# Performance work log

Hardware: AMD Instinct MI355X
Metric: run time of the kernel (lower is better)

The kernel has to match this reference:

```python
import math
import jax, jax.numpy as jnp
import numpy as np

B, Q, L, H = 32, 40, 1024, 1024
WINDOW_FRAMES, MAX_V_L = 16, 1024
MAX_DELTA = 0.1
NUM_PASSES = 2


def setup_inputs() -> dict:
    key = jax.random.key(0)
    ks = jax.random.split(key, 8)
    init_log_sigma = math.log(WINDOW_FRAMES / (2.0 * MAX_V_L))
    return {
        "pred_spans": jax.random.uniform(ks[0], (B, Q, 2), dtype=jnp.float32),
        "vid_feat": jax.random.normal(ks[1], (B, L, H), dtype=jnp.float32),
        "vid_mask": jnp.ones((B, L), dtype=jnp.float32),
        "txt_rep": jax.random.normal(ks[2], (B, H), dtype=jnp.float32),
        "log_sigma_start": jnp.float32(init_log_sigma),
        "log_sigma_end": jnp.float32(init_log_sigma),
        "sigma_width_scale_start": jnp.float32(0.01),
        "sigma_width_scale_end": jnp.float32(-0.01),
        "txt_proj_w": jax.random.normal(ks[3], (H, 2), dtype=jnp.float32) * 0.02,
        "txt_proj_b": jnp.zeros((2,), dtype=jnp.float32),
        "mlp0_w": jax.random.normal(ks[4], (3 * H, H), dtype=jnp.float32) * (1.0 / math.sqrt(3 * H)),
        "mlp0_b": jnp.zeros((H,), dtype=jnp.float32),
        "mlp1_w": jax.random.normal(ks[5], (H, 2), dtype=jnp.float32) * (1.0 / math.sqrt(H)),
        "mlp1_b": jnp.zeros((2,), dtype=jnp.float32),
    }


def reference(pred_spans, vid_feat, vid_mask, txt_rep,
              log_sigma_start, log_sigma_end,
              sigma_width_scale_start, sigma_width_scale_end,
              txt_proj_w, txt_proj_b, mlp0_w, mlp0_b, mlp1_w, mlp1_b):
    b, q, _ = pred_spans.shape
    l = vid_feat.shape[1]
    # span (center,width) -> (start,end) in [0,1]
    start = jnp.clip(pred_spans[..., 0] - pred_spans[..., 1] / 2, 0.0, 1.0)  # (B,Q)
    end = jnp.clip(pred_spans[..., 0] + pred_spans[..., 1] / 2, 0.0, 1.0)
    t_pos = jnp.linspace(0.0, 1.0, l)  # (L,)
    min_sig = 1.0 / (4.0 * l)
    log_range = math.log(max(float(l) * min_sig * 4.0, 1.0 + 1e-6))
    # semantic sigma offsets (B,2)
    txt_off = jnp.tanh(txt_rep @ txt_proj_w + txt_proj_b) * (0.5 * log_range)
    txt_off_s, txt_off_e = txt_off[:, 0:1], txt_off[:, 1:2]  # (B,1)
    txt_expand = jnp.broadcast_to(txt_rep[:, None, :], (b, q, txt_rep.shape[-1]))
    mask = vid_mask[:, None, :]  # (B,1,L)

    def _pool(anchor, sigma):
        # Gaussian soft-attention pooling over frames; anchor,sigma: (B,Q)
        dist2 = ((t_pos[None, None, :] - anchor[:, :, None]) / sigma[:, :, None]) ** 2
        w = jnp.exp(-0.5 * dist2) * mask  # (B,Q,L)
        w = w / jnp.maximum(jnp.sum(w, -1, keepdims=True), 1e-8)
        return jnp.einsum('bql,blh->bqh', w, vid_feat)

    passes = []
    for _ in range(NUM_PASSES):
        width = jnp.maximum(end - start, 1e-6)  # (B,Q)
        sig_s = jnp.maximum(jnp.exp(log_sigma_start + sigma_width_scale_start * width + txt_off_s), min_sig)
        sig_e = jnp.maximum(jnp.exp(log_sigma_end + sigma_width_scale_end * width + txt_off_e), min_sig)
        start_feat = _pool(start, sig_s)
        end_feat = _pool(end, sig_e)
        joint = jnp.concatenate([start_feat, end_feat, txt_expand], axis=-1)  # (B,Q,3H)
        hidden = jax.nn.relu(joint @ mlp0_w + mlp0_b)
        deltas = jnp.tanh(hidden @ mlp1_w + mlp1_b) * MAX_DELTA  # (B,Q,2)
        start = jnp.clip(start + deltas[..., 0], 0.0, 1.0)
        end = jnp.clip(end + deltas[..., 1], 0.0, 1.0)
        center_r = (start + end) / 2.0
        width_r = jnp.maximum(end - start, 1e-6)
        passes.append(jnp.stack([center_r, width_r], axis=-1))
    return passes[-1], jnp.stack(passes, axis=0)
```

## Files before the change

kernel.cpp:

```cpp
#include <hip/hip_runtime.h>

#define B_   32
#define Q_   40
#define L_   1024
#define H_   1024
#define QQ_  80
#define M_   1280
#define K3_  3072
#define JK_  2048

#define OB_W0T   0u
#define OB_WT2   6291456u
#define OB_JOINT 11534336u
#define OB_PART  16777216u
#define OB_TXTB  27262976u
#define OB_TXTP  27328512u
#define OB_MISC  27590656u
#define MS_START 0
#define MS_END   1280
#define MS_TOS   2560
#define MS_TOE   2592

typedef short bf8 __attribute__((ext_vector_type(8)));
typedef short bf4 __attribute__((ext_vector_type(4)));
typedef float f4  __attribute__((ext_vector_type(4)));

static __device__ __forceinline__ unsigned short f2b(float f) {
    unsigned int x = __float_as_uint(f);
    unsigned int r = x + 0x7FFFu + ((x >> 16) & 1u);
    return (unsigned short)(r >> 16);
}
static __device__ __forceinline__ unsigned int pk2(float lo, float hi) {
    return (unsigned int)f2b(lo) | ((unsigned int)f2b(hi) << 16);
}
static __device__ __forceinline__ float b2f16(unsigned short u) {
    return __uint_as_float((unsigned int)u << 16);
}
static __device__ __forceinline__ float blo(unsigned int u) {
    return __uint_as_float(u << 16);
}
static __device__ __forceinline__ float bhi(unsigned int u) {
    return __uint_as_float(u & 0xffff0000u);
}

static __device__ __forceinline__ void block_reduce2(float& a, float& b, float* scr) {
    #pragma unroll
    for (int off = 32; off > 0; off >>= 1) {
        a += __shfl_down(a, off);
        b += __shfl_down(b, off);
    }
    int wv = threadIdx.x >> 6, lane = threadIdx.x & 63;
    __syncthreads();
    if (lane == 0) { scr[wv] = a; scr[4 + wv] = b; }
    __syncthreads();
    a = scr[0] + scr[1] + scr[2] + scr[3];
    b = scr[4] + scr[5] + scr[6] + scr[7];
}

__global__ __launch_bounds__(256) void k_setup(const float* __restrict__ w0,
                                               unsigned short* __restrict__ w0t,
                                               const float* __restrict__ txt,
                                               const float* __restrict__ pw,
                                               const float* __restrict__ pb,
                                               const float* __restrict__ spans,
                                               unsigned short* __restrict__ txtb,
                                               float* __restrict__ msc) {
    int z = blockIdx.z, tid = threadIdx.x;
    if (z == 3) {
        int flat = blockIdx.x * 16 + blockIdx.y;
        if (flat < B_) {
            int b = flat;
            int h4 = tid * 4;
            float4 tv = *(const float4*)(txt + (size_t)b * H_ + h4);
            float4 pa = *(const float4*)(pw + 2 * h4);
            float4 pc = *(const float4*)(pw + 2 * h4 + 4);
            float s0 = tv.x * pa.x + tv.y * pa.z + tv.z * pc.x + tv.w * pc.z;
            float s1 = tv.x * pa.y + tv.y * pa.w + tv.z * pc.y + tv.w * pc.w;
            ushort4 o;
            o.x = f2b(tv.x); o.y = f2b(tv.y); o.z = f2b(tv.z); o.w = f2b(tv.w);
            *(ushort4*)(txtb + (size_t)b * H_ + h4) = o;
            __shared__ float scr[8];
            block_reduce2(s0, s1, scr);
            if (tid == 0) {
                const float half_lr = 4.9999975e-07f;
                msc[MS_TOS + b] = tanhf(s0 + pb[0]) * half_lr;
                msc[MS_TOE + b] = tanhf(s1 + pb[1]) * half_lr;
            }
        } else if (flat < 37) {
            int i = (flat - B_) * 256 + tid;
            if (i < M_) {
                float c = spans[2 * i], w = spans[2 * i + 1];
                msc[MS_START + i] = fminf(fmaxf(c - 0.5f * w, 0.f), 1.f);
                msc[MS_END + i]   = fminf(fmaxf(c + 0.5f * w, 0.f), 1.f);
            }
        }
        return;
    }
    __shared__ float tile[64][69];
    const float* s = w0 + (size_t)z * 1024 * H_;
    unsigned short* d = w0t + (size_t)z * 1024;
    int r0 = blockIdx.x * 64, c0 = blockIdx.y * 64;
    int col4 = (tid & 15) * 4, row = tid >> 4;
    #pragma unroll
    for (int it = 0; it < 4; it++) {
        int r = it * 16 + row;
        float4 v = *(const float4*)(s + (size_t)(r0 + r) * 1024 + c0 + col4);
        *(float4*)(&tile[r][col4]) = v;
    }
    __syncthreads();
    #pragma unroll
    for (int it = 0; it < 2; it++) {
        int slot = it * 256 + tid;
        int c = slot >> 3, chunk = slot & 7;
        int r = chunk * 8;
        uint4 vv;
        vv.x = (unsigned int)f2b(tile[r + 0][c]) | ((unsigned int)f2b(tile[r + 1][c]) << 16);
        vv.y = (unsigned int)f2b(tile[r + 2][c]) | ((unsigned int)f2b(tile[r + 3][c]) << 16);
        vv.z = (unsigned int)f2b(tile[r + 4][c]) | ((unsigned int)f2b(tile[r + 5][c]) << 16);
        vv.w = (unsigned int)f2b(tile[r + 6][c]) | ((unsigned int)f2b(tile[r + 7][c]) << 16);
        *(uint4*)(d + (size_t)(c0 + c) * K3_ + r0 + r) = vv;
    }
}

static __device__ __forceinline__ void weights_body(int m, float s, float e,
                                                    const float* __restrict__ vmask,
                                                    float ls_s, float ls_e,
                                                    float sw_s, float sw_e,
                                                    const float* __restrict__ msc,
                                                    unsigned short* __restrict__ wt2,
                                                    float* scr) {
    int b = m / Q_, q = m - b * Q_;
    int tid = threadIdx.x;
    float width = fmaxf(e - s, 1e-6f);
    const float min_sig = 1.0f / (4.0f * (float)L_);
    float sig_s = fmaxf(expf(ls_s + sw_s * width + msc[MS_TOS + b]), min_sig);
    float sig_e = fmaxf(expf(ls_e + sw_e * width + msc[MS_TOE + b]), min_sig);
    float inv_s = 1.0f / sig_s, inv_e = 1.0f / sig_e;

    float wsv[4], wev[4], sumS = 0.f, sumE = 0.f;
    #pragma unroll
    for (int k = 0; k < 4; k++) {
        int l = tid + k * 256;
        float t = (float)l * (1.0f / 1023.0f);
        float mk = vmask[b * L_ + l];
        float ds = (t - s) * inv_s, de = (t - e) * inv_e;
        float a = expf(-0.5f * ds * ds) * mk;
        float c = expf(-0.5f * de * de) * mk;
        wsv[k] = a; wev[k] = c; sumS += a; sumE += c;
    }
    block_reduce2(sumS, sumE, scr);
    float iS = 1.0f / fmaxf(sumS, 1e-8f);
    float iE = 1.0f / fmaxf(sumE, 1e-8f);
    unsigned short* wq = wt2 + ((size_t)b * QQ_ + q) * L_;
    unsigned short* we = wt2 + ((size_t)b * QQ_ + Q_ + q) * L_;
    #pragma unroll
    for (int k = 0; k < 4; k++) {
        int l = tid + k * 256;
        wq[l] = f2b(wsv[k] * iS);
        we[l] = f2b(wev[k] * iE);
    }
}

__global__ __launch_bounds__(256) void k_stage2(const float* __restrict__ vmask,
                                                const float* __restrict__ p_ls_s,
                                                const float* __restrict__ p_ls_e,
                                                const float* __restrict__ p_sw_s,
                                                const float* __restrict__ p_sw_e,
                                                const float* __restrict__ msc,
                                                unsigned short* __restrict__ wt2,
                                                const unsigned short* __restrict__ txtb,
                                                const unsigned short* __restrict__ w0t,
                                                unsigned short* __restrict__ txtp) {
    int bid = blockIdx.x;
    if (bid < M_) {
        __shared__ float scr[8];
        int m = bid;
        weights_body(m, msc[MS_START + m], msc[MS_END + m], vmask,
                     p_ls_s[0], p_ls_e[0], p_sw_s[0], p_sw_e[0], msc, wt2, scr);
        return;
    }
    int t = bid - M_;
    int nIdx = t & 15, mIdx = (t >> 4) & 1, kIdx = t >> 5;
    int wv = threadIdx.x >> 6, lane = threadIdx.x & 63;
    int ml = lane & 15, kg = lane >> 4;
    int mbase = mIdx * 16;
    int nbase = nIdx * 64 + wv * 16;
    int kz = kIdx * 256;
    const unsigned short* ap = txtb + ((size_t)(mbase + ml) * H_ + kz + kg * 8);
    const unsigned short* bp = w0t + ((size_t)(nbase + ml) * K3_ + JK_ + kz + kg * 8);
    f4 acc = (f4){0.f, 0.f, 0.f, 0.f};
    #pragma unroll
    for (int k0 = 0; k0 < 256; k0 += 32) {
        bf8 a = *(const bf8*)(ap + k0);
        bf8 bb = *(const bf8*)(bp + k0);
        acc = __builtin_amdgcn_mfma_f32_16x16x32_bf16(a, bb, acc, 0, 0, 0);
    }
    unsigned short* pp = txtp + (size_t)kIdx * B_ * H_;
    int n = nbase + ml;
    #pragma unroll
    for (int r = 0; r < 4; r++) {
        int m = mbase + kg * 4 + r;
        pp[(size_t)m * H_ + n] = f2b(acc[r]);
    }
}

__global__ __launch_bounds__(256) void k_pool_mfma(const float* __restrict__ vid,
                                                   const unsigned short* __restrict__ wt2,
                                                   unsigned short* __restrict__ joint) {
    int b = blockIdx.x, ht = blockIdx.y;
    int tid = threadIdx.x;
    int hsub = tid >> 6, lane = tid & 63;
    int ml = lane & 15, kg = lane >> 4;
    int h0 = ht * 64;

    __shared__ __align__(16) unsigned short tb[2][4096];
    __shared__ __align__(16) unsigned short ta[2][80 * 72];

    int l0 = tid >> 3;
    int h8 = (tid & 7) * 8;
    int sB = (l0 >> 2) & 1, kgB = l0 >> 3, lrB = l0 & 3;
    int h16 = h8 >> 4, hc = h8 & 15;
    int b_off = ((((h16) * 2 + sB) * 4 + kgB) * 64) + lrB * 16 + hc;
    const float* vbase = vid + (size_t)b * L_ * H_ + h0 + h8;

    const unsigned short* awsrc = wt2 + (size_t)b * QQ_ * L_;

    f4 acc[5];
    #pragma unroll
    for (int t = 0; t < 5; t++) acc[t] = (f4){0.f, 0.f, 0.f, 0.f};

    float4 pv0, pv1, pv2, pv3;
    uint4 av0, av1, av2;

    auto issueB = [&](int c) {
        const float* src = vbase + (size_t)(c * 64 + l0) * H_;
        pv0 = *(const float4*)(src);
        pv1 = *(const float4*)(src + 4);
        pv2 = *(const float4*)(src + 32 * H_);
        pv3 = *(const float4*)(src + 32 * H_ + 4);
    };
    auto issueA = [&](int c) {
        int i0 = tid, i1 = tid + 256;
        av0 = *(const uint4*)(awsrc + (size_t)(i0 >> 3) * L_ + c * 64 + (i0 & 7) * 8);
        av1 = *(const uint4*)(awsrc + (size_t)(i1 >> 3) * L_ + c * 64 + (i1 & 7) * 8);
        if (tid < 128) {
            int i2 = tid + 512;
            av2 = *(const uint4*)(awsrc + (size_t)(i2 >> 3) * L_ + c * 64 + (i2 & 7) * 8);
        }
    };
    auto writeStage = [&](int buf) {
        uint4 w;
        w.x = pk2(pv0.x, pv0.y); w.y = pk2(pv0.z, pv0.w);
        w.z = pk2(pv1.x, pv1.y); w.w = pk2(pv1.z, pv1.w);
        *(uint4*)(&tb[buf][b_off]) = w;
        uint4 w2;
        w2.x = pk2(pv2.x, pv2.y); w2.y = pk2(pv2.z, pv2.w);
        w2.z = pk2(pv3.x, pv3.y); w2.w = pk2(pv3.z, pv3.w);
        *(uint4*)(&tb[buf][b_off + 2048]) = w2;
        int i0 = tid, i1 = tid + 256;
        *(uint4*)(&ta[buf][(i0 >> 3) * 72 + (i0 & 7) * 8]) = av0;
        *(uint4*)(&ta[buf][(i1 >> 3) * 72 + (i1 & 7) * 8]) = av1;
        if (tid < 128) {
            int i2 = tid + 512;
            *(uint4*)(&ta[buf][(i2 >> 3) * 72 + (i2 & 7) * 8]) = av2;
        }
    };

    issueB(0); issueA(0);
    writeStage(0);
    __syncthreads();

    for (int c = 0; c < 16; c++) {
        int buf = c & 1;
        if (c < 15) { issueB(c + 1); issueA(c + 1); }

        #pragma unroll
        for (int s2 = 0; s2 < 2; s2++) {
            unsigned trb = (unsigned)(uintptr_t)(&tb[buf][0]) + (s2 * 4 + hsub) * 1024
                           + lane * 8;
            bf4 lo, hi;
            asm volatile("ds_read_b64_tr_b16 %0, %2\n\t"
                         "ds_read_b64_tr_b16 %1, %2 offset:512\n\t"
                         "s_waitcnt lgkmcnt(0)"
                         : "=v"(lo), "=v"(hi)
                         : "v"(trb));
            __builtin_amdgcn_sched_barrier(0);
            bf8 bfrag = __builtin_shufflevector(lo, hi, 0, 1, 2, 3, 4, 5, 6, 7);
            #pragma unroll
            for (int t = 0; t < 5; t++) {
                bf8 afr = *(const bf8*)(&ta[buf][(t * 16 + ml) * 72 + s2 * 32 + kg * 8]);
                acc[t] = __builtin_amdgcn_mfma_f32_16x16x32_bf16(afr, bfrag, acc[t], 0, 0, 0);
            }
        }

        if (c < 15) writeStage(buf ^ 1);
        __syncthreads();
    }

    #pragma unroll
    for (int t = 0; t < 5; t++) {
        #pragma unroll
        for (int r = 0; r < 4; r++) {
            int qq = t * 16 + kg * 4 + r;
            int row = b * Q_ + (qq >= Q_ ? qq - Q_ : qq);
            int col = (qq >= Q_ ? H_ : 0) + h0 + hsub * 16 + ml;
            joint[(size_t)row * JK_ + col] = f2b(acc[t][r]);
        }
    }
}

__global__ __launch_bounds__(256) void k_mlp0_mfma(const unsigned short* __restrict__ joint,
                                                   const unsigned short* __restrict__ w0t,
                                                   const unsigned short* __restrict__ txtp,
                                                   unsigned short* __restrict__ part) {
    int wv = threadIdx.x >> 6, lane = threadIdx.x & 63;
    int ml = lane & 15, kg = lane >> 4;
    int mbase = blockIdx.x * 64 + wv * 16;
    int nbase = blockIdx.y * 64;
    int kbase = blockIdx.z * 512;
    const unsigned short* ap = joint + ((size_t)(mbase + ml) * JK_ + kbase + kg * 8);
    const unsigned short* bp = w0t + ((size_t)(nbase + ml) * K3_ + kbase + kg * 8);
    f4 acc[4];
    #pragma unroll
    for (int t = 0; t < 4; t++) acc[t] = (f4){0.f, 0.f, 0.f, 0.f};

    #pragma unroll 4
    for (int k0 = 0; k0 < 512; k0 += 32) {
        bf8 a = *(const bf8*)(ap + k0);
        #pragma unroll
        for (int t = 0; t < 4; t++) {
            bf8 bb = *(const bf8*)(bp + (size_t)t * 16 * K3_ + k0);
            acc[t] = __builtin_amdgcn_mfma_f32_16x16x32_bf16(a, bb, acc[t], 0, 0, 0);
        }
    }
    const unsigned short* tp = txtp + (size_t)blockIdx.z * B_ * H_;
    unsigned short* pp = part + (size_t)blockIdx.z * M_ * H_;
    #pragma unroll
    for (int t = 0; t < 4; t++) {
        int n = nbase + t * 16 + ml;
        #pragma unroll
        for (int r = 0; r < 4; r++) {
            int m = mbase + kg * 4 + r;
            int b = m / Q_;
            float v = acc[t][r] + b2f16(tp[(size_t)b * H_ + n]);
            pp[(size_t)m * H_ + n] = f2b(v);
        }
    }
}

__global__ __launch_bounds__(256) void k_mlp1w(const float* __restrict__ w1,
                                               const float* __restrict__ b0,
                                               const float* __restrict__ b1,
                                               const unsigned short* __restrict__ part,
                                               float* __restrict__ msc,
                                               float* __restrict__ out, int pass,
                                               int do_weights,
                                               const float* __restrict__ vmask,
                                               const float* __restrict__ p_ls_s,
                                               const float* __restrict__ p_ls_e,
                                               const float* __restrict__ p_sw_s,
                                               const float* __restrict__ p_sw_e,
                                               unsigned short* __restrict__ wt2) {
    int m = blockIdx.x, tid = threadIdx.x;
    int k4 = tid * 4;
    float4 bb = *(const float4*)(b0 + k4);
    float h0 = bb.x, h1 = bb.y, h2 = bb.z, h3 = bb.w;
    #pragma unroll
    for (int z = 0; z < 4; z++) {
        uint2 u = *(const uint2*)(part + (size_t)z * M_ * H_ + (size_t)m * H_ + k4);
        h0 += blo(u.x); h1 += bhi(u.x);
        h2 += blo(u.y); h3 += bhi(u.y);
    }
    h0 = fmaxf(h0, 0.f); h1 = fmaxf(h1, 0.f);
    h2 = fmaxf(h2, 0.f); h3 = fmaxf(h3, 0.f);
    float4 wa = *(const float4*)(w1 + 2 * k4);
    float4 wb = *(const float4*)(w1 + 2 * k4 + 4);
    float p0 = h0 * wa.x + h1 * wa.z + h2 * wb.x + h3 * wb.z;
    float p1 = h0 * wa.y + h1 * wa.w + h2 * wb.y + h3 * wb.w;

    __shared__ float scr[8];
    __shared__ float sh_s, sh_e;
    block_reduce2(p0, p1, scr);
    if (tid == 0) {
        float d0 = tanhf(p0 + b1[0]) * 0.1f;
        float d1 = tanhf(p1 + b1[1]) * 0.1f;
        float s = fminf(fmaxf(msc[MS_START + m] + d0, 0.f), 1.f);
        float e = fminf(fmaxf(msc[MS_END + m] + d1, 0.f), 1.f);
        msc[MS_START + m] = s;
        msc[MS_END + m] = e;
        sh_s = s; sh_e = e;
        float cen = 0.5f * (s + e);
        float wid = fmaxf(e - s, 1e-6f);
        out[2560 + (size_t)(pass * M_ + m) * 2 + 0] = cen;
        out[2560 + (size_t)(pass * M_ + m) * 2 + 1] = wid;
        if (pass == 1) { out[2 * m + 0] = cen; out[2 * m + 1] = wid; }
    }
    __syncthreads();
    if (do_weights) {
        weights_body(m, sh_s, sh_e, vmask,
                     p_ls_s[0], p_ls_e[0], p_sw_s[0], p_sw_e[0], msc, wt2, scr);
    }
}

extern "C" void kernel_launch(void* const* d_in, const int* in_sizes, int n_in,
                              void* d_out, int out_size, void* d_ws, size_t ws_size,
                              hipStream_t stream) {
    const float* spans = (const float*)d_in[0];
    const float* vid   = (const float*)d_in[1];
    const float* vmask = (const float*)d_in[2];
    const float* txt   = (const float*)d_in[3];
    const float* ls_s  = (const float*)d_in[4];
    const float* ls_e  = (const float*)d_in[5];
    const float* sw_s  = (const float*)d_in[6];
    const float* sw_e  = (const float*)d_in[7];
    const float* pw    = (const float*)d_in[8];
    const float* pb    = (const float*)d_in[9];
    const float* w0    = (const float*)d_in[10];
    const float* b0    = (const float*)d_in[11];
    const float* w1    = (const float*)d_in[12];
    const float* b1    = (const float*)d_in[13];
    char* wsb = (char*)d_ws;
    unsigned short* w0t   = (unsigned short*)(wsb + OB_W0T);
    unsigned short* wt2   = (unsigned short*)(wsb + OB_WT2);
    unsigned short* joint = (unsigned short*)(wsb + OB_JOINT);
    unsigned short* part  = (unsigned short*)(wsb + OB_PART);
    unsigned short* txtb  = (unsigned short*)(wsb + OB_TXTB);
    unsigned short* txtp  = (unsigned short*)(wsb + OB_TXTP);
    float* msc = (float*)(wsb + OB_MISC);
    float* out = (float*)d_out;

    hipLaunchKernelGGL(k_setup, dim3(16, 16, 4), dim3(256), 0, stream,
                       w0, w0t, txt, pw, pb, spans, txtb, msc);
    hipLaunchKernelGGL(k_stage2, dim3(M_ + 128), dim3(256), 0, stream,
                       vmask, ls_s, ls_e, sw_s, sw_e, msc, wt2, txtb, w0t, txtp);
    for (int p = 0; p < 2; p++) {
        hipLaunchKernelGGL(k_pool_mfma, dim3(B_, 16), dim3(256), 0, stream, vid, wt2, joint);
        hipLaunchKernelGGL(k_mlp0_mfma, dim3(20, 16, 4), dim3(256), 0, stream,
                           joint, w0t, txtp, part);
        hipLaunchKernelGGL(k_mlp1w, dim3(M_), dim3(256), 0, stream,
                           w1, b0, b1, part, msc, out, p, (p == 0) ? 1 : 0,
                           vmask, ls_s, ls_e, sw_s, sw_e, wt2);
    }
}
```

Measured before the change: 365.1 us.

## Fold stage2 into setup and first pool launch to drop a kernel

Removes the separate k_stage2 launch. The first-pass Gaussian weight computation moves into k_setup as extra z-slices, which recompute the text projection and span clipping locally. The txt@W0 partial GEMM moves into extra blockIdx.y rows of the first pool launch. This saves one launch and its serialization point, at the cost of redundant per-block text projection work and heavier setup and pool grids. Correctness depends on w0t and txtb being written by the earlier setup launch.

```diff
diff --git a/kernel.cpp b/kernel.cpp
--- a/kernel.cpp
+++ b/kernel.cpp
@@ -57,6 +57,57 @@
     b = scr[4] + scr[5] + scr[6] + scr[7];
 }
 
+static __device__ __forceinline__ void weights_core(int m, float s, float e,
+                                                    float toff_s, float toff_e,
+                                                    const float* __restrict__ vmask,
+                                                    float ls_s, float ls_e,
+                                                    float sw_s, float sw_e,
+                                                    unsigned short* __restrict__ wt2,
+                                                    float* scr) {
+    int b = m / Q_, q = m - b * Q_;
+    int tid = threadIdx.x;
+    float width = fmaxf(e - s, 1e-6f);
+    const float min_sig = 1.0f / (4.0f * (float)L_);
+    float sig_s = fmaxf(expf(ls_s + sw_s * width + toff_s), min_sig);
+    float sig_e = fmaxf(expf(ls_e + sw_e * width + toff_e), min_sig);
+    float inv_s = 1.0f / sig_s, inv_e = 1.0f / sig_e;
+
+    float wsv[4], wev[4], sumS = 0.f, sumE = 0.f;
+    #pragma unroll
+    for (int k = 0; k < 4; k++) {
+        int l = tid + k * 256;
+        float t = (float)l * (1.0f / 1023.0f);
+        float mk = vmask[b * L_ + l];
+        float ds = (t - s) * inv_s, de = (t - e) * inv_e;
+        float a = expf(-0.5f * ds * ds) * mk;
+        float c = expf(-0.5f * de * de) * mk;
+        wsv[k] = a; wev[k] = c; sumS += a; sumE += c;
+    }
+    block_reduce2(sumS, sumE, scr);
+    float iS = 1.0f / fmaxf(sumS, 1e-8f);
+    float iE = 1.0f / fmaxf(sumE, 1e-8f);
+    unsigned short* wq = wt2 + ((size_t)b * QQ_ + q) * L_;
+    unsigned short* we = wt2 + ((size_t)b * QQ_ + Q_ + q) * L_;
+    #pragma unroll
+    for (int k = 0; k < 4; k++) {
+        int l = tid + k * 256;
+        wq[l] = f2b(wsv[k] * iS);
+        we[l] = f2b(wev[k] * iE);
+    }
+}
+
+static __device__ __forceinline__ void weights_body(int m, float s, float e,
+                                                    const float* __restrict__ vmask,
+                                                    float ls_s, float ls_e,
+                                                    float sw_s, float sw_e,
+                                                    const float* __restrict__ msc,
+                                                    unsigned short* __restrict__ wt2,
+                                                    float* scr) {
+    int b = m / Q_;
+    weights_core(m, s, e, msc[MS_TOS + b], msc[MS_TOE + b],
+                 vmask, ls_s, ls_e, sw_s, sw_e, wt2, scr);
+}
+
 __global__ __launch_bounds__(256) void k_setup(const float* __restrict__ w0,
                                                unsigned short* __restrict__ w0t,
                                                const float* __restrict__ txt,
@@ -64,8 +115,35 @@
                                                const float* __restrict__ pb,
                                                const float* __restrict__ spans,
                                                unsigned short* __restrict__ txtb,
-                                               float* __restrict__ msc) {
+                                               float* __restrict__ msc,
+                                               const float* __restrict__ vmask,
+                                               const float* __restrict__ p_ls_s,
+                                               const float* __restrict__ p_ls_e,
+                                               const float* __restrict__ p_sw_s,
+                                               const float* __restrict__ p_sw_e,
+                                               unsigned short* __restrict__ wt2) {
     int z = blockIdx.z, tid = threadIdx.x;
+    if (z >= 4) {
+        int m = (z - 4) * 256 + (blockIdx.x * 16 + blockIdx.y);
+        int b = m / Q_;
+        int h4 = tid * 4;
+        float4 tv = *(const float4*)(txt + (size_t)b * H_ + h4);
+        float4 pa = *(const float4*)(pw + 2 * h4);
+        float4 pc = *(const float4*)(pw + 2 * h4 + 4);
+        float s0 = tv.x * pa.x + tv.y * pa.z + tv.z * pc.x + tv.w * pc.z;
+        float s1 = tv.x * pa.y + tv.y * pa.w + tv.z * pc.y + tv.w * pc.w;
+        __shared__ float scrW[8];
+        block_reduce2(s0, s1, scrW);
+        const float half_lr = 4.9999975e-07f;
+        float toff_s = tanhf(s0 + pb[0]) * half_lr;
+        float toff_e = tanhf(s1 + pb[1]) * half_lr;
+        float c = spans[2 * m], w = spans[2 * m + 1];
+        float s = fminf(fmaxf(c - 0.5f * w, 0.f), 1.f);
+        float e = fminf(fmaxf(c + 0.5f * w, 0.f), 1.f);
+        weights_core(m, s, e, toff_s, toff_e, vmask,
+                     p_ls_s[0], p_ls_e[0], p_sw_s[0], p_sw_e[0], wt2, scrW);
+        return;
+    }
     if (z == 3) {
         int flat = blockIdx.x * 16 + blockIdx.y;
         if (flat < B_) {
@@ -122,91 +200,39 @@
     }
 }
 
-static __device__ __forceinline__ void weights_body(int m, float s, float e,
-                                                    const float* __restrict__ vmask,
-                                                    float ls_s, float ls_e,
-                                                    float sw_s, float sw_e,
-                                                    const float* __restrict__ msc,
-                                                    unsigned short* __restrict__ wt2,
-                                                    float* scr) {
-    int b = m / Q_, q = m - b * Q_;
-    int tid = threadIdx.x;
-    float width = fmaxf(e - s, 1e-6f);
-    const float min_sig = 1.0f / (4.0f * (float)L_);
-    float sig_s = fmaxf(expf(ls_s + sw_s * width + msc[MS_TOS + b]), min_sig);
-    float sig_e = fmaxf(expf(ls_e + sw_e * width + msc[MS_TOE + b]), min_sig);
-    float inv_s = 1.0f / sig_s, inv_e = 1.0f / sig_e;
-
-    float wsv[4], wev[4], sumS = 0.f, sumE = 0.f;
-    #pragma unroll
-    for (int k = 0; k < 4; k++) {
-        int l = tid + k * 256;
-        float t = (float)l * (1.0f / 1023.0f);
-        float mk = vmask[b * L_ + l];
-        float ds = (t - s) * inv_s, de = (t - e) * inv_e;
-        float a = expf(-0.5f * ds * ds) * mk;
-        float c = expf(-0.5f * de * de) * mk;
-        wsv[k] = a; wev[k] = c; sumS += a; sumE += c;
-    }
-    block_reduce2(sumS, sumE, scr);
-    float iS = 1.0f / fmaxf(sumS, 1e-8f);
-    float iE = 1.0f / fmaxf(sumE, 1e-8f);
-    unsigned short* wq = wt2 + ((size_t)b * QQ_ + q) * L_;
-    unsigned short* we = wt2 + ((size_t)b * QQ_ + Q_ + q) * L_;
-    #pragma unroll
-    for (int k = 0; k < 4; k++) {
-        int l = tid + k * 256;
-        wq[l] = f2b(wsv[k] * iS);
-        we[l] = f2b(wev[k] * iE);
-    }
-}
-
-__global__ __launch_bounds__(256) void k_stage2(const float* __restrict__ vmask,
-                                                const float* __restrict__ p_ls_s,
-                                                const float* __restrict__ p_ls_e,
-                                                const float* __restrict__ p_sw_s,
-                                                const float* __restrict__ p_sw_e,
-                                                const float* __restrict__ msc,
-                                                unsigned short* __restrict__ wt2,
-                                                const unsigned short* __restrict__ txtb,
-                                                const unsigned short* __restrict__ w0t,
-                                                unsigned short* __restrict__ txtp) {
-    int bid = blockIdx.x;
-    if (bid < M_) {
-        __shared__ float scr[8];
-        int m = bid;
-        weights_body(m, msc[MS_START + m], msc[MS_END + m], vmask,
-                     p_ls_s[0], p_ls_e[0], p_sw_s[0], p_sw_e[0], msc, wt2, scr);
-        return;
-    }
-    int t = bid - M_;
-    int nIdx = t & 15, mIdx = (t >> 4) & 1, kIdx = t >> 5;
-    int wv = threadIdx.x >> 6, lane = threadIdx.x & 63;
-    int ml = lane & 15, kg = lane >> 4;
-    int mbase = mIdx * 16;
-    int nbase = nIdx * 64 + wv * 16;
-    int kz = kIdx * 256;
-    const unsigned short* ap = txtb + ((size_t)(mbase + ml) * H_ + kz + kg * 8);
-    const unsigned short* bp = w0t + ((size_t)(nbase + ml) * K3_ + JK_ + kz + kg * 8);
-    f4 acc = (f4){0.f, 0.f, 0.f, 0.f};
-    #pragma unroll
-    for (int k0 = 0; k0 < 256; k0 += 32) {
-        bf8 a = *(const bf8*)(ap + k0);
-        bf8 bb = *(const bf8*)(bp + k0);
-        acc = __builtin_amdgcn_mfma_f32_16x16x32_bf16(a, bb, acc, 0, 0, 0);
-    }
-    unsigned short* pp = txtp + (size_t)kIdx * B_ * H_;
-    int n = nbase + ml;
-    #pragma unroll
-    for (int r = 0; r < 4; r++) {
-        int m = mbase + kg * 4 + r;
-        pp[(size_t)m * H_ + n] = f2b(acc[r]);
-    }
-}
-
 __global__ __launch_bounds__(256) void k_pool_mfma(const float* __restrict__ vid,
                                                    const unsigned short* __restrict__ wt2,
-                                                   unsigned short* __restrict__ joint) {
+                                                   unsigned short* __restrict__ joint,
+                                                   const unsigned short* __restrict__ txtb,
+                                                   const unsigned short* __restrict__ w0t,
+                                                   unsigned short* __restrict__ txtp) {
+    if (blockIdx.y >= 16) {
+        int t = (blockIdx.y - 16) * 32 + blockIdx.x;
+        int nIdx = t & 15, mIdx = (t >> 4) & 1, kIdx = t >> 5;
+        int wv = threadIdx.x >> 6, lane = threadIdx.x & 63;
+        int ml = lane & 15, kg = lane >> 4;
+        int mbase = mIdx * 16;
+        int nbase = nIdx * 64 + wv * 16;
+        int kz = kIdx * 256;
+        const unsigned short* ap = txtb + ((size_t)(mbase + ml) * H_ + kz + kg * 8);
+        const unsigned short* bp = w0t + ((size_t)(nbase + ml) * K3_ + JK_ + kz + kg * 8);
+        f4 acc = (f4){0.f, 0.f, 0.f, 0.f};
+        #pragma unroll
+        for (int k0 = 0; k0 < 256; k0 += 32) {
+            bf8 a = *(const bf8*)(ap + k0);
+            bf8 bb = *(const bf8*)(bp + k0);
+            acc = __builtin_amdgcn_mfma_f32_16x16x32_bf16(a, bb, acc, 0, 0, 0);
+        }
+        unsigned short* pp = txtp + (size_t)kIdx * B_ * H_;
+        int n = nbase + ml;
+        #pragma unroll
+        for (int r = 0; r < 4; r++) {
+            int m = mbase + kg * 4 + r;
+            pp[(size_t)m * H_ + n] = f2b(acc[r]);
+        }
+        return;
+    }
+
     int b = blockIdx.x, ht = blockIdx.y;
     int tid = threadIdx.x;
     int hsub = tid >> 6, lane = tid & 63;
@@ -429,12 +455,12 @@
     float* msc = (float*)(wsb + OB_MISC);
     float* out = (float*)d_out;
 
-    hipLaunchKernelGGL(k_setup, dim3(16, 16, 4), dim3(256), 0, stream,
-                       w0, w0t, txt, pw, pb, spans, txtb, msc);
-    hipLaunchKernelGGL(k_stage2, dim3(M_ + 128), dim3(256), 0, stream,
-                       vmask, ls_s, ls_e, sw_s, sw_e, msc, wt2, txtb, w0t, txtp);
+    hipLaunchKernelGGL(k_setup, dim3(16, 16, 9), dim3(256), 0, stream,
+                       w0, w0t, txt, pw, pb, spans, txtb, msc,
+                       vmask, ls_s, ls_e, sw_s, sw_e, wt2);
     for (int p = 0; p < 2; p++) {
-        hipLaunchKernelGGL(k_pool_mfma, dim3(B_, 16), dim3(256), 0, stream, vid, wt2, joint);
+        hipLaunchKernelGGL(k_pool_mfma, dim3(B_, (p == 0) ? 20 : 16), dim3(256), 0, stream,
+                           vid, wt2, joint, txtb, w0t, txtp);
         hipLaunchKernelGGL(k_mlp0_mfma, dim3(20, 16, 4), dim3(256), 0, stream,
                            joint, w0t, txtp, part);
         hipLaunchKernelGGL(k_mlp1w, dim3(M_), dim3(256), 0, stream,
```

After: 361.1 us. About the same (-1.1%).
